# Kernel optimization log

Hardware: AMD Instinct MI355X
Metric: run time of the kernel (lower is better)

Reference implementation:

```python
import jax, jax.numpy as jnp
import numpy as np

B, L, PRED = 32, 1024, 256
CIN = 32            # enc_in == dec_in == c_out
DM, DFF, H, M = 512, 2048, 8, 64
E = DM // H
EL, DL = 2, 1
K = 25              # moving-avg kernel


def moving_avg(x):
    # torch: replicate-pad (K-1)//2 on both ends, then AvgPool1d(K, stride=1)
    pad = (K - 1) // 2
    xp = jnp.concatenate([jnp.repeat(x[:, :1], pad, axis=1), x, jnp.repeat(x[:, -1:], pad, axis=1)], axis=1)
    cs = jnp.cumsum(xp, axis=1)
    cs = jnp.concatenate([jnp.zeros_like(cs[:, :1]), cs], axis=1)
    return (cs[:, K:] - cs[:, :-K]) / K


def decomp(x):
    ma = moving_avg(x)
    return x - ma, ma


def circ_conv3(x, W):
    # Conv1d(kernel=3, padding=1, padding_mode='circular', bias=False); x:[B,L,C], W:[O,C,3]
    xp = jnp.concatenate([x[:, -1:], x, x[:, :1]], axis=1)
    win = jnp.stack([xp[:, :-2], xp[:, 1:-1], xp[:, 2:]], axis=-1)  # [B,L,C,3]
    return jnp.einsum('blcj,ocj->blo', win, W)


def pos_emb():
    pos = jnp.arange(L, dtype=jnp.float32)[:, None]
    div = jnp.exp(jnp.arange(0, DM, 2, dtype=jnp.float32) * (-np.log(10000.0) / DM))
    pe = jnp.zeros((L, DM), dtype=jnp.float32)
    pe = pe.at[:, 0::2].set(jnp.sin(pos * div))
    pe = pe.at[:, 1::2].set(jnp.cos(pos * div))
    return pe


def fourier_self(q, k, v, w):
    # FourierBlock: rFFT over time, keep lowest M modes, per-(head,mode) complex matmul, irFFT
    Bq, Lq = q.shape[0], q.shape[1]
    xft = jnp.fft.rfft(q.transpose(0, 2, 3, 1), axis=-1)[..., :M]        # [B,H,E,M]
    wc = w[..., 0] + 1j * w[..., 1]                                      # [H,E,E,M]
    om = jnp.einsum('bhem,heom->bhom', xft, wc)
    out_ft = jnp.zeros((Bq, H, E, Lq // 2 + 1), dtype=om.dtype).at[..., :M].set(om)
    return jnp.fft.irfft(out_ft, n=Lq, axis=-1).transpose(0, 3, 1, 2)    # [B,L,H,E]


def fourier_cross(q, k, v, w):
    # FourierCrossAttention (activation='tanh'); note official code uses k-modes as values
    Bq, Lq = q.shape[0], q.shape[1]
    xq = jnp.fft.rfft(q.transpose(0, 2, 3, 1), axis=-1)[..., :M]         # [B,H,E,M]
    xk = jnp.fft.rfft(k.transpose(0, 2, 3, 1), axis=-1)[..., :M]
    qk = jnp.tanh(jnp.einsum('bhex,bhey->bhxy', xq, xk))                 # complex tanh
    qkv = jnp.einsum('bhxy,bhey->bhex', qk, xk)
    wc = w[..., 0] + 1j * w[..., 1]
    om = jnp.einsum('bhex,heox->bhox', qkv, wc)
    out_ft = jnp.zeros((Bq, H, E, Lq // 2 + 1), dtype=om.dtype).at[..., :M].set(om)
    return jnp.fft.irfft(out_ft / (DM * DM), n=Lq, axis=-1).transpose(0, 3, 1, 2)


def mha(xq, xkv, Wq, bq, Wk, bk, Wv, bv, Wo, bo, inner, fw):
    Bq, Lq = xq.shape[0], xq.shape[1]
    q = (xq @ Wq.T + bq).reshape(Bq, Lq, H, E)
    k = (xkv @ Wk.T + bk).reshape(Bq, -1, H, E)
    v = (xkv @ Wv.T + bv).reshape(Bq, -1, H, E)
    o = inner(q, k, v, fw).reshape(Bq, Lq, DM)
    return o @ Wo.T + bo


def setup_inputs():
    ks = iter(jax.random.split(jax.random.key(0), 80))
    p = lambda shape: jax.random.normal(next(ks), shape, dtype=jnp.float32) * 0.02
    z = lambda shape: jnp.zeros(shape, dtype=jnp.float32)
    d = {}
    d['x_enc'] = jax.random.normal(next(ks), (B, L, CIN), dtype=jnp.float32)
    d['tok_W'] = p((DM, CIN, 3))
    for pre, n in (('enc_', EL), ('dec_s', DL), ('dec_c', DL)):
        for nm in ('Wq', 'Wk', 'Wv', 'Wo'):
            d[pre + nm] = p((n, DM, DM))
        for nm in ('bq', 'bk', 'bv', 'bo'):
            d[pre + nm] = z((n, DM))
    d['enc_c1W'] = p((EL, DFF, DM)); d['enc_c1b'] = z((EL, DFF))
    d['enc_c2W'] = p((EL, DM, DFF)); d['enc_c2b'] = z((EL, DM))
    d['dec_c1W'] = p((DL, DFF, DM)); d['dec_c1b'] = z((DL, DFF))
    d['dec_c2W'] = p((DL, DM, DFF)); d['dec_c2b'] = z((DL, DM))
    d['dec_trW'] = p((DL, CIN, DM, 3))
    d['fb_enc'] = p((H, E, E, M, 2))
    d['fb_dec'] = p((H, E, E, M, 2))
    d['fc_w'] = p((H, E, E, M, 2))
    d['p1W'] = p((CIN, CIN)); d['p1b'] = z((CIN,))
    d['p2W'] = p((PRED, L)); d['p2b'] = z((PRED,))
    d['p3W'] = p((CIN, DM)); d['p3b'] = z((CIN,))
    return d


def reference(x_enc, tok_W, enc_Wq, enc_Wk, enc_Wv, enc_Wo, enc_bq, enc_bk, enc_bv, enc_bo,
              dec_sWq, dec_sWk, dec_sWv, dec_sWo, dec_sbq, dec_sbk, dec_sbv, dec_sbo,
              dec_cWq, dec_cWk, dec_cWv, dec_cWo, dec_cbq, dec_cbk, dec_cbv, dec_cbo,
              enc_c1W, enc_c1b, enc_c2W, enc_c2b, dec_c1W, dec_c1b, dec_c2W, dec_c2b,
              dec_trW, fb_enc, fb_dec, fc_w, p1W, p1b, p2W, p2b, p3W, p3b):
    seasonal_init, trend_init = decomp(x_enc)
    enc = circ_conv3(x_enc, tok_W) + pos_emb()[None]   # DataEmbedding (eval: no dropout)
    for l in range(EL):
        h = enc + mha(enc, enc, enc_Wq[l], enc_bq[l], enc_Wk[l], enc_bk[l], enc_Wv[l], enc_bv[l],
                      enc_Wo[l], enc_bo[l], fourier_self, fb_enc)
        h, _ = decomp(h)
        y = jax.nn.relu(h @ enc_c1W[l].T + enc_c1b[l]) @ enc_c2W[l].T + enc_c2b[l]
        enc, _ = decomp(h + y)
    # NB: top-level source calls decoder(enc_out, enc_out, ...): dec_embedding output is unused
    x = enc
    trend = trend_init
    for l in range(DL):
        x = x + mha(x, x, dec_sWq[l], dec_sbq[l], dec_sWk[l], dec_sbk[l], dec_sWv[l], dec_sbv[l],
                    dec_sWo[l], dec_sbo[l], fourier_self, fb_dec)
        x, t1 = decomp(x)
        x = x + mha(x, enc, dec_cWq[l], dec_cbq[l], dec_cWk[l], dec_cbk[l], dec_cWv[l], dec_cbv[l],
                    dec_cWo[l], dec_cbo[l], fourier_cross, fc_w)
        x, t2 = decomp(x)
        y = jax.nn.relu(x @ dec_c1W[l].T + dec_c1b[l]) @ dec_c2W[l].T + dec_c2b[l]
        x, t3 = decomp(x + y)
        trend = trend + circ_conv3(t1 + t2 + t3, dec_trW[l])   # trend projection (circular conv3)
    out = trend + (x @ p3W.T + p3b)                            # [B,L,CIN]
    out = out @ p1W.T + p1b
    out = jnp.einsum('blc,pl->bpc', out, p2W) + p2b[None, :, None]  # proj2 over time -> [B,PRED,CIN]
    return out
```

## Files before the change

kernel.cpp:

```cpp
#include <hip/hip_runtime.h>
#include <math.h>

namespace {

constexpr int cB = 32, cL = 1024, cCIN = 32, cDM = 512, cDFF = 2048;
constexpr int cH = 8, cE = 64, cM = 64, cPRED = 256;
constexpr int M2 = 2 * cM;

typedef __attribute__((ext_vector_type(8))) short short8v;
typedef __attribute__((ext_vector_type(4))) float float4v;

__device__ inline unsigned short f2bf(float f) {
  unsigned int u = __builtin_bit_cast(unsigned int, f);
  u += 0x7FFFu + ((u >> 16) & 1u);
  return (unsigned short)(u >> 16);
}
__device__ inline float bf2f(unsigned short s) {
  return __builtin_bit_cast(float, (unsigned int)s << 16);
}

typedef const __attribute__((address_space(1))) unsigned int gu32_t;
typedef __attribute__((address_space(3))) unsigned int lu32_t;
__device__ inline void gld16(const void* g, void* l) {
  __builtin_amdgcn_global_load_lds((gu32_t*)g, (lu32_t*)l, 16, 0, 0);
}

__global__ void basis_kernel(short* __restrict__ basisdb, short* __restrict__ basisib) {
  int idx = blockIdx.x * 256 + threadIdx.x;
  if (idx >= M2 * cL) return;
  int t = idx & (cL - 1);
  int m2 = idx >> 10;
  int m = m2 >> 1;
  float ang = 6.2831853071795864f * (float)((m * t) & (cL - 1)) / (float)cL;
  float cv = cosf(ang), sv = sinf(ang);
  float vd = (m2 & 1) ? -sv : cv;
  basisdb[idx] = (short)f2bf(vd);
  float s = (m == 0) ? ((m2 & 1) ? 0.f : (1.f / (float)cL)) : (2.f / (float)cL);
  basisib[t * M2 + m2] = (short)f2bf(vd * s);
}

__global__ void pe_kernel(float* __restrict__ pe) {
  int idx = blockIdx.x * 256 + threadIdx.x;
  int o = idx & (cDM - 1), t = idx >> 9;
  int i = o >> 1;
  float freq = __expf((float)(2 * i) * (-9.210340371976184f / (float)cDM));
  float ang = freq * (float)t;
  pe[idx] = (o & 1) ? cosf(ang) : sinf(ang);
}

constexpr int NJOB = 14;
struct CvtArgs {
  const float* src[NJOB];
  short* dst[NJOB];
  int n[NJOB];
};
__global__ void cvtm_kernel(CvtArgs a) {
  int j = blockIdx.y;
  const float* s = a.src[j];
  short* d = a.dst[j];
  int n = a.n[j];
  for (int i = blockIdx.x * 256 + threadIdx.x; i < n; i += gridDim.x * 256)
    d[i] = (short)f2bf(s[i]);
}

__global__ void prep_kernel(const float* __restrict__ tok_W, const float* __restrict__ trW,
                            const float* __restrict__ p3W, const float* __restrict__ p3b,
                            short* __restrict__ Bpadb, short* __restrict__ Wtr3b,
                            short* __restrict__ p3padb, float* __restrict__ p3bpadf) {
  int idx = blockIdx.x * 256 + threadIdx.x;
  if (idx < 512 * 128) {
    int o = idx >> 7, s = idx & 127, j = s >> 5, c = s & 31;
    Bpadb[idx] = (j < 3) ? (short)f2bf(tok_W[o * 96 + c * 3 + j]) : (short)0;
  }
  if (idx < 128 * 1536) {
    int o = idx / 1536, r = idx % 1536, j = r >> 9, c = r & 511;
    Wtr3b[idx] = (o < 32) ? (short)f2bf(trW[(long)o * 1536 + c * 3 + j]) : (short)0;
  }
  if (idx < 128 * 512) {
    int o = idx >> 9, k = idx & 511;
    p3padb[idx] = (o < 32) ? (short)f2bf(p3W[o * 512 + k]) : (short)0;
  }
  if (idx < 128) p3bpadf[idx] = (idx < 32) ? p3b[idx] : 0.f;
}

__global__ void winbuild_kernel(const float* __restrict__ x, short* __restrict__ win) {
  int idx = blockIdx.x * 256 + threadIdx.x;
  int s4 = idx & 31;
  int row = idx >> 5;
  int t = row & (cL - 1), b = row >> 10;
  int j = s4 >> 3, c4 = s4 & 7;
  unsigned int lo = 0, hi = 0;
  if (j < 3) {
    int ts = (t + j + cL - 1) & (cL - 1);
    float4 v = *(const float4*)&x[((long)b * cL + ts) * cCIN + c4 * 4];
    lo = (unsigned int)f2bf(v.x) | ((unsigned int)f2bf(v.y) << 16);
    hi = (unsigned int)f2bf(v.z) | ((unsigned int)f2bf(v.w) << 16);
  }
  *(uint2*)&win[row * 128 + s4 * 4] = make_uint2(lo, hi);
}

__global__ __launch_bounds__(256) void transpose_bf(const short* __restrict__ in,
                                                    short* __restrict__ out) {
  __shared__ short tile[32][33];
  int b = blockIdx.z;
  in += (long)b * cL * cDM;
  out += (long)b * cL * cDM;
  int c0 = blockIdx.x * 32, t0 = blockIdx.y * 32;
  int tx = threadIdx.x & 31, ty = threadIdx.x >> 5;
#pragma unroll
  for (int r = 0; r < 32; r += 8) tile[ty + r][tx] = in[(long)(t0 + ty + r) * cDM + c0 + tx];
  __syncthreads();
#pragma unroll
  for (int r = 0; r < 32; r += 8)
    out[(long)(c0 + ty + r) * cL + t0 + tx] = tile[tx][ty + r];
}

__global__ void decomp_kernel(const float* __restrict__ x, float* __restrict__ maf, int n8,
                              int C) {
  int idx = blockIdx.x * 256 + threadIdx.x;
  if (idx >= n8) return;
  int c = idx % C;
  int u = idx / C;
  int t0 = (u & 127) * 8;
  int b = u >> 7;
  long base = (long)b * cL * C + c;
  float s = 0.f;
#pragma unroll
  for (int j = -12; j <= 12; j++) {
    int tt = t0 + j;
    tt = tt < 0 ? 0 : (tt >= cL ? cL - 1 : tt);
    s += x[base + (long)tt * C];
  }
#pragma unroll
  for (int k = 0; k < 8; k++) {
    int t = t0 + k;
    maf[base + (long)t * C] = s * (1.0f / 25.0f);
    int ta = t + 13;
    ta = ta >= cL ? cL - 1 : ta;
    int td = t - 12;
    td = td < 0 ? 0 : td;
    s += x[base + (long)ta * C] - x[base + (long)td * C];
  }
}

__global__ void decompb_kernel(const short* __restrict__ x, short* __restrict__ sb,
                               short* __restrict__ mab, int maacc, int n8, int C) {
  int idx = blockIdx.x * 256 + threadIdx.x;
  if (idx >= n8) return;
  int c = idx % C;
  int u = idx / C;
  int t0 = (u & 127) * 8;
  int b = u >> 7;
  long base = (long)b * cL * C + c;
  float s = 0.f;
#pragma unroll
  for (int j = -12; j <= 12; j++) {
    int tt = t0 + j;
    tt = tt < 0 ? 0 : (tt >= cL ? cL - 1 : tt);
    s += bf2f((unsigned short)x[base + (long)tt * C]);
  }
#pragma unroll
  for (int k = 0; k < 8; k++) {
    int t = t0 + k;
    long e = base + (long)t * C;
    float ma = s * (1.0f / 25.0f);
    if (sb) sb[e] = (short)f2bf(bf2f((unsigned short)x[e]) - ma);
    if (mab) {
      float v = maacc ? bf2f((unsigned short)mab[e]) + ma : ma;
      mab[e] = (short)f2bf(v);
    }
    int ta = t + 13;
    ta = ta >= cL ? cL - 1 : ta;
    int td = t - 12;
    td = td < 0 ? 0 : td;
    s += bf2f((unsigned short)x[base + (long)ta * C]) - bf2f((unsigned short)x[base + (long)td * C]);
  }
}

__global__ __launch_bounds__(256) void p2_kernel(const float* __restrict__ x,
                                                 const float* __restrict__ W,
                                                 const float* __restrict__ bias,
                                                 float* __restrict__ out) {
  __shared__ float tile[256 * 32];
  int b = blockIdx.x;
  int p0 = blockIdx.y * 8;
  int c = threadIdx.x & 31, pl = threadIdx.x >> 5;
  const float* xb = x + (long)b * cL * cCIN;
  const float* w = W + (long)(p0 + pl) * cL;
  float s = 0.f;
  for (int l0 = 0; l0 < cL; l0 += 256) {
    __syncthreads();
    for (int i = threadIdx.x; i < 256 * 32; i += 256) tile[i] = xb[(long)l0 * 32 + i];
    __syncthreads();
#pragma unroll 8
    for (int l = 0; l < 256; l++) s += tile[l * 32 + c] * w[l0 + l];
  }
  out[((long)b * cPRED + p0 + pl) * cCIN + c] = s + bias[p0 + pl];
}

__global__ __launch_bounds__(512) void modemix_t_kernel(const float* __restrict__ F,
                                                        const unsigned short* __restrict__ W,
                                                        short* __restrict__ Gt, float scale) {
  int b = blockIdx.x, h = blockIdx.y;
  __shared__ float2 Fs[cE][cM];
  __shared__ short ot[128][72];
  const float* Fb = F + ((long)b * cDM + h * cE) * M2;
  for (int i = threadIdx.x; i < cE * cM; i += 512) {
    int e = i >> 6, x = i & 63;
    Fs[e][x] = ((const float2*)(Fb + (long)e * M2))[x];
  }
  __syncthreads();
  int x = threadIdx.x & 63, og = threadIdx.x >> 6;
  float2 acc[8];
#pragma unroll
  for (int i = 0; i < 8; i++) acc[i] = make_float2(0.f, 0.f);
  for (int e = 0; e < cE; e++) {
    float2 f = Fs[e][x];
#pragma unroll
    for (int i = 0; i < 8; i++) {
      int o = og * 8 + i;
      unsigned int wu = *(const unsigned int*)&W[((((long)h * cE + e) * cE + o) * cM + x) * 2];
      float wx = bf2f((unsigned short)wu), wy = bf2f((unsigned short)(wu >> 16));
      acc[i].x += f.x * wx - f.y * wy;
      acc[i].y += f.x * wy + f.y * wx;
    }
  }
#pragma unroll
  for (int i = 0; i < 8; i++) {
    int o = og * 8 + i;
    ot[2 * x][o] = (short)f2bf(acc[i].x * scale);
    ot[2 * x + 1][o] = (short)f2bf(acc[i].y * scale);
  }
  __syncthreads();
  short* gb = Gt + (long)b * (M2 * cDM) + h * cE;
  for (int u = threadIdx.x; u < 1024; u += 512) {
    int row = u >> 3, seg = u & 7;
    *(uint4*)&gb[(long)row * cDM + seg * 8] = *(const uint4*)&ot[row][seg * 8];
  }
}

__global__ __launch_bounds__(1024) void fused_cross_kernel(const float* __restrict__ Fq,
                                                           const float* __restrict__ Fk,
                                                           const unsigned short* __restrict__ W,
                                                           short* __restrict__ Gt, float scale) {
  __shared__ __align__(16) char smem[65536];
  float2(*KsT)[cE] = (float2(*)[cE])smem;
  float2(*qks)[cM] = (float2(*)[cM])(smem + 32768);
  int b = blockIdx.x, h = blockIdx.y;
  const float* kb = Fk + ((long)b * cDM + h * cE) * M2;
  for (int i = threadIdx.x; i < cE * cM; i += 1024) {
    int e = i >> 6, y = i & 63;
    KsT[y][e] = ((const float2*)(kb + (long)e * M2))[y];
  }
  __syncthreads();
  {
    int x = threadIdx.x & 63, yg = threadIdx.x >> 6;
    const float* qb = Fq + ((long)b * cDM + h * cE) * M2;
    float2 acc[4];
#pragma unroll
    for (int i = 0; i < 4; i++) acc[i] = make_float2(0.f, 0.f);
    for (int e = 0; e < cE; e++) {
      float2 q = ((const float2*)(qb + (long)e * M2))[x];
#pragma unroll
      for (int i = 0; i < 4; i++) {
        float2 k = KsT[yg * 4 + i][e];
        acc[i].x += q.x * k.x - q.y * k.y;
        acc[i].y += q.x * k.y + q.y * k.x;
      }
    }
#pragma unroll
    for (int i = 0; i < 4; i++) {
      int y = yg * 4 + i;
      float a = acc[i].x, bi = acc[i].y;
      float re, im;
      float t2a = 2.f * a;
      if (fabsf(t2a) > 60.f) {
        re = t2a > 0.f ? 1.f : -1.f;
        im = 0.f;
      } else {
        float denom = coshf(t2a) + cosf(2.f * bi);
        re = sinhf(t2a) / denom;
        im = sinf(2.f * bi) / denom;
      }
      qks[y][x] = make_float2(re, im);
    }
  }
  __syncthreads();
  int e = threadIdx.x & 63, xg = threadIdx.x >> 6;
  float2 a2[4];
#pragma unroll
  for (int i = 0; i < 4; i++) a2[i] = make_float2(0.f, 0.f);
  for (int y = 0; y < cM; y++) {
    float2 k = KsT[y][e];
#pragma unroll
    for (int i = 0; i < 4; i++) {
      float2 qk = qks[y][xg * 4 + i];
      a2[i].x += qk.x * k.x - qk.y * k.y;
      a2[i].y += qk.x * k.y + qk.y * k.x;
    }
  }
  __syncthreads();
  float2(*Qv)[cM] = (float2(*)[cM])smem;
#pragma unroll
  for (int i = 0; i < 4; i++) Qv[e][xg * 4 + i] = a2[i];
  __syncthreads();
  {
    int x = threadIdx.x & 63, og = threadIdx.x >> 6;
    float2 m[4];
#pragma unroll
    for (int i = 0; i < 4; i++) m[i] = make_float2(0.f, 0.f);
    for (int ee = 0; ee < cE; ee++) {
      float2 f = Qv[ee][x];
#pragma unroll
      for (int i = 0; i < 4; i++) {
        int o = og * 4 + i;
        unsigned int wu = *(const unsigned int*)&W[((((long)h * cE + ee) * cE + o) * cM + x) * 2];
        float wx = bf2f((unsigned short)wu), wy = bf2f((unsigned short)(wu >> 16));
        m[i].x += f.x * wx - f.y * wy;
        m[i].y += f.x * wy + f.y * wx;
      }
    }
    short(*ot)[72] = (short(*)[72])(smem + 32768);
#pragma unroll
    for (int i = 0; i < 4; i++) {
      int o = og * 4 + i;
      ot[2 * x][o] = (short)f2bf(m[i].x * scale);
      ot[2 * x + 1][o] = (short)f2bf(m[i].y * scale);
    }
    __syncthreads();
    short* gb = Gt + (long)b * (M2 * cDM) + h * cE;
    int u = threadIdx.x;
    {
      int row = u >> 3, seg = u & 7;
      *(uint4*)&gb[(long)row * cDM + seg * 8] =
          *(const uint4*)&((short(*)[72])(smem + 32768))[row][seg * 8];
    }
  }
}

constexpr int GBM = 128, GBN = 128, GBK = 16, LPAD = 132;

__global__ __launch_bounds__(256) void gemm_kernel(const float* __restrict__ A,
                                                   const float* __restrict__ B,
                                                   const float* __restrict__ bias,
                                                   float* __restrict__ C, int M, int N, int K) {
  __shared__ float As[GBK][LPAD];
  __shared__ float Bs[GBK][LPAD];
  int n0 = blockIdx.x * GBN, m0 = blockIdx.y * GBM;
  int tid = threadIdx.x;
  int tx = tid & 15, ty = tid >> 4;
  float acc[8][8];
#pragma unroll
  for (int i = 0; i < 8; i++)
#pragma unroll
    for (int j = 0; j < 8; j++) acc[i][j] = 0.f;

  for (int k0 = 0; k0 < K; k0 += GBK) {
#pragma unroll
    for (int p = 0; p < 8; p++) {
      int i = p * 256 + tid;
      int mm = i >> 4, kk = i & 15;
      int gm = m0 + mm;
      As[kk][mm] = (gm < M && k0 + kk < K) ? A[(long)gm * K + k0 + kk] : 0.f;
    }
#pragma unroll
    for (int p = 0; p < 8; p++) {
      int i = p * 256 + tid;
      int nn = i >> 4, kk = i & 15;
      int gn = n0 + nn;
      Bs[kk][nn] = (gn < N && k0 + kk < K) ? B[(long)gn * K + k0 + kk] : 0.f;
    }
    __syncthreads();
#pragma unroll
    for (int kk = 0; kk < GBK; kk++) {
      float a[8], bb[8];
      *(float4*)&a[0] = *(const float4*)&As[kk][ty * 8];
      *(float4*)&a[4] = *(const float4*)&As[kk][ty * 8 + 4];
      *(float4*)&bb[0] = *(const float4*)&Bs[kk][tx * 8];
      *(float4*)&bb[4] = *(const float4*)&Bs[kk][tx * 8 + 4];
#pragma unroll
      for (int i = 0; i < 8; i++)
#pragma unroll
        for (int j = 0; j < 8; j++) acc[i][j] += a[i] * bb[j];
    }
    __syncthreads();
  }

  for (int i = 0; i < 8; i++) {
    int gm = m0 + ty * 8 + i;
    if (gm >= M) break;
    long rowoff = (long)gm * N;
    for (int j = 0; j < 8; j++) {
      int gn = n0 + tx * 8 + j;
      if (gn < N) C[rowoff + gn] = acc[i][j] + (bias ? bias[gn] : 0.f);
    }
  }
}

__global__ __launch_bounds__(256) void mfma_gemm_bf(
    const short* __restrict__ A, const short* __restrict__ B, const float* __restrict__ bias,
    const float* __restrict__ addend, const short* __restrict__ addendb,
    const float* __restrict__ pe, const float* __restrict__ m0b, float* __restrict__ Cf,
    short* __restrict__ Cb, int M, int N, int K, int lda, long sA, long sB, long sC, int relu,
    int Nreal, int ldc, int amode) {
  __shared__ __align__(16) short As[8192];
  __shared__ __align__(16) short Bs[8192];
  int nwg = gridDim.x * gridDim.y * gridDim.z;
  int orig = blockIdx.x + gridDim.x * (blockIdx.y + gridDim.y * blockIdx.z);
  int q = nwg >> 3, r = nwg & 7;
  int xcd = orig & 7, ii = orig >> 3;
  int flat = (xcd < r ? xcd * (q + 1) : r * (q + 1) + (xcd - r) * q) + ii;
  int bx = flat % (int)gridDim.x;
  int tmp = flat / (int)gridDim.x;
  int by = tmp % (int)gridDim.y;
  int bz = tmp / (int)gridDim.y;

  int z = bz;
  A += (long)z * sA;
  B += (long)z * sB;
  if (Cf) Cf += (long)z * sC;
  if (Cb) Cb += (long)z * sC;
  const float* Ad = addend ? addend + (long)z * sC : nullptr;
  const short* Adb = addendb ? addendb + (long)z * sC : nullptr;
  int n0 = bx * 128, m0 = by * 128;
  int tid = threadIdx.x;
  int lane = tid & 63;
  int w = tid >> 6;
  int wm = w & 1, wn = w >> 1;
  int lr = lane & 15, lg = lane >> 4;
  int lrow = lane >> 3;
  int scol = ((lane & 7) * 8) ^ (lrow << 3);

  float4v acc[4][4];
#pragma unroll
  for (int i = 0; i < 4; i++)
#pragma unroll
    for (int j = 0; j < 4; j++) acc[i][j] = (float4v){0.f, 0.f, 0.f, 0.f};

  auto stage = [&](int k0) {
#pragma unroll
    for (int j = 0; j < 4; j++) {
      int seg = w * 4 + j;
      int row = seg * 8 + lrow;
      const short* ga;
      if (amode == 0) {
        ga = A + (long)(m0 + row) * lda + k0 + scol;
      } else {
        int r2 = m0 + row;
        int bb = r2 >> 10, t = r2 & 1023;
        int jj = k0 >> 9, c0 = k0 & 511;
        ga = A + ((((long)(bb << 10)) | ((t + jj + 1023) & 1023)) << 9) + c0 + scol;
      }
      gld16(ga, &As[seg * 512]);
      const short* gb = B + (long)(n0 + row) * K + k0 + scol;
      gld16(gb, &Bs[seg * 512]);
    }
  };

  int nk = K >> 6;
  int swr = (lr & 7) << 3;
  for (int t = 0; t < nk; ++t) {
    stage(t << 6);
    asm volatile("s_waitcnt vmcnt(0)" ::: "memory");
    __syncthreads();
#pragma unroll
    for (int ks = 0; ks < 2; ks++) {
      short8v af[4], bfr[4];
#pragma unroll
      for (int mi = 0; mi < 4; mi++)
        af[mi] = *(const short8v*)&As[(wm * 64 + mi * 16 + lr) * 64 + ((ks * 32 + lg * 8) ^ swr)];
#pragma unroll
      for (int ni = 0; ni < 4; ni++)
        bfr[ni] = *(const short8v*)&Bs[(wn * 64 + ni * 16 + lr) * 64 + ((ks * 32 + lg * 8) ^ swr)];
#pragma unroll
      for (int mi = 0; mi < 4; mi++)
#pragma unroll
        for (int ni = 0; ni < 4; ni++)
          acc[mi][ni] =
              __builtin_amdgcn_mfma_f32_16x16x32_bf16(af[mi], bfr[ni], acc[mi][ni], 0, 0, 0);
    }
    __syncthreads();
  }

#pragma unroll
  for (int mi = 0; mi < 4; mi++) {
#pragma unroll
    for (int i = 0; i < 4; i++) {
      int gr = m0 + wm * 64 + mi * 16 + lg * 4 + i;
      long rowoff = (long)gr * ldc;
#pragma unroll
      for (int ni = 0; ni < 4; ni++) {
        int gc = n0 + wn * 64 + ni * 16 + lr;
        if (gc < Nreal) {
          float v = acc[mi][ni][i];
          if (bias) v += bias[gc];
          if (pe) v += pe[((gr & (cL - 1)) << 9) + gc];
          if (m0b && gc == 0) v += 1024.f * m0b[gr];
          if (Ad) v += Ad[rowoff + gc];
          if (Adb) v += bf2f((unsigned short)Adb[rowoff + gc]);
          if (relu) v = fmaxf(v, 0.f);
          if (Cf) Cf[rowoff + gc] = v;
          if (Cb) Cb[rowoff + gc] = (short)f2bf(v);
        }
      }
    }
  }
}

__global__ __launch_bounds__(256) void mfma_gemm64(
    const short* __restrict__ A, const short* __restrict__ B, const float* __restrict__ bias,
    const float* __restrict__ addf, const short* __restrict__ addb,
    const float* __restrict__ m0b, float* __restrict__ Cf, short* __restrict__ Cb, int M, int N,
    int K, int lda, long sA, long sB, long sC, int Nreal, int ldc, int amode,
    const short* __restrict__ A2, const short* __restrict__ B2, const float* __restrict__ m0b2,
    float* __restrict__ Cf2, int zsplit) {
  __shared__ __align__(16) short As[4096];
  __shared__ __align__(16) short Bs[4096];
  int nwg = gridDim.x * gridDim.y * gridDim.z;
  int orig = blockIdx.x + gridDim.x * (blockIdx.y + gridDim.y * blockIdx.z);
  int q = nwg >> 3, r = nwg & 7;
  int xcd = orig & 7, ii = orig >> 3;
  int flat = (xcd < r ? xcd * (q + 1) : r * (q + 1) + (xcd - r) * q) + ii;
  int bx = flat % (int)gridDim.x;
  int tmp = flat / (int)gridDim.x;
  int by = tmp % (int)gridDim.y;
  int bz = tmp / (int)gridDim.y;

  int z = bz;
  if (zsplit > 0 && bz >= zsplit) {
    A = A2;
    B = B2;
    m0b = m0b2;
    Cf = Cf2;
    z = bz - zsplit;
  }
  A += (long)z * sA;
  B += (long)z * sB;
  if (Cf) Cf += (long)z * sC;
  if (Cb) Cb += (long)z * sC;
  const float* Ad = addf ? addf + (long)z * sC : nullptr;
  const short* Adb = addb ? addb + (long)z * sC : nullptr;
  int n0 = bx * 64, m0 = by * 64;
  int tid = threadIdx.x;
  int lane = tid & 63;
  int w = tid >> 6;
  int wm = w & 1, wn = w >> 1;
  int lr = lane & 15, lg = lane >> 4;
  int lrow = lane >> 3;
  int scol = ((lane & 7) * 8) ^ (lrow << 3);

  float4v acc[2][2];
#pragma unroll
  for (int i = 0; i < 2; i++)
#pragma unroll
    for (int j = 0; j < 2; j++) acc[i][j] = (float4v){0.f, 0.f, 0.f, 0.f};

  int nk = K >> 6;
  int swr = (lr & 7) << 3;
  for (int t = 0; t < nk; ++t) {
    int k0 = t << 6;
#pragma unroll
    for (int j = 0; j < 2; j++) {
      int seg = w * 2 + j;
      int row = seg * 8 + lrow;
      const short* ga;
      if (amode == 0) {
        ga = A + (long)(m0 + row) * lda + k0 + scol;
      } else {
        int r2 = m0 + row;
        int bb = r2 >> 10, tt = r2 & 1023;
        int jj = k0 >> 9, c0 = k0 & 511;
        ga = A + ((((long)(bb << 10)) | ((tt + jj + 1023) & 1023)) << 9) + c0 + scol;
      }
      gld16(ga, &As[seg * 512]);
      gld16(B + (long)(n0 + row) * K + k0 + scol, &Bs[seg * 512]);
    }
    asm volatile("s_waitcnt vmcnt(0)" ::: "memory");
    __syncthreads();
#pragma unroll
    for (int ks = 0; ks < 2; ks++) {
      short8v af[2], bfr[2];
#pragma unroll
      for (int mi = 0; mi < 2; mi++)
        af[mi] = *(const short8v*)&As[(wm * 32 + mi * 16 + lr) * 64 + ((ks * 32 + lg * 8) ^ swr)];
#pragma unroll
      for (int ni = 0; ni < 2; ni++)
        bfr[ni] = *(const short8v*)&Bs[(wn * 32 + ni * 16 + lr) * 64 + ((ks * 32 + lg * 8) ^ swr)];
#pragma unroll
      for (int mi = 0; mi < 2; mi++)
#pragma unroll
        for (int ni = 0; ni < 2; ni++)
          acc[mi][ni] =
              __builtin_amdgcn_mfma_f32_16x16x32_bf16(af[mi], bfr[ni], acc[mi][ni], 0, 0, 0);
    }
    __syncthreads();
  }

#pragma unroll
  for (int mi = 0; mi < 2; mi++) {
#pragma unroll
    for (int i = 0; i < 4; i++) {
      int gr = m0 + wm * 32 + mi * 16 + lg * 4 + i;
      long rowoff = (long)gr * ldc;
#pragma unroll
      for (int ni = 0; ni < 2; ni++) {
        int gc = n0 + wn * 32 + ni * 16 + lr;
        if (gc < Nreal) {
          float v = acc[mi][ni][i];
          if (bias) v += bias[gc];
          if (m0b && gc == 0) v += 1024.f * m0b[gr];
          if (Ad) v += Ad[rowoff + gc];
          if (Adb) v += bf2f((unsigned short)Adb[rowoff + gc]);
          if (Cf) Cf[rowoff + gc] = v;
          if (Cb) Cb[rowoff + gc] = (short)f2bf(v);
        }
      }
    }
  }
}

}

extern "C" void kernel_launch(void* const* d_in, const int* in_sizes, int n_in, void* d_out,
                              int out_size, void* d_ws, size_t ws_size, hipStream_t stream) {
  const float* x_enc = (const float*)d_in[0];
  const float* tok_W = (const float*)d_in[1];
  const float* enc_Wq = (const float*)d_in[2];
  const float* enc_Wo = (const float*)d_in[5];
  const float* enc_bq = (const float*)d_in[6];
  const float* enc_bo = (const float*)d_in[9];
  const float* dsWq = (const float*)d_in[10];
  const float* dsWo = (const float*)d_in[13];
  const float* dsbq = (const float*)d_in[14];
  const float* dsbo = (const float*)d_in[17];
  const float* dcWq = (const float*)d_in[18];
  const float* dcWk = (const float*)d_in[19];
  const float* dcWo = (const float*)d_in[21];
  const float* dcbq = (const float*)d_in[22];
  const float* dcbk = (const float*)d_in[23];
  const float* dcbo = (const float*)d_in[25];
  const float* enc_c1W = (const float*)d_in[26];
  const float* enc_c1b = (const float*)d_in[27];
  const float* enc_c2W = (const float*)d_in[28];
  const float* enc_c2b = (const float*)d_in[29];
  const float* dec_c1W = (const float*)d_in[30];
  const float* dec_c1b = (const float*)d_in[31];
  const float* dec_c2W = (const float*)d_in[32];
  const float* dec_c2b = (const float*)d_in[33];
  const float* dec_trW = (const float*)d_in[34];
  const float* fb_enc = (const float*)d_in[35];
  const float* fb_dec = (const float*)d_in[36];
  const float* fc_w = (const float*)d_in[37];
  const float* p1W = (const float*)d_in[38];
  const float* p1b = (const float*)d_in[39];
  const float* p2W = (const float*)d_in[40];
  const float* p2b = (const float*)d_in[41];
  const float* p3W = (const float*)d_in[42];
  const float* p3b = (const float*)d_in[43];

  constexpr long MIXW = 8L * 64 * 64 * 64 * 2;

  auto layout_bytes = [&](long BG, long RH) -> size_t {
    size_t t = 0;
    auto add = [&](size_t b) { t = (t + b + 255) & ~(size_t)255; };
    add(2 * 262144 * 2); add(2 * 262144 * 2);
    add(262144 * 2); add(262144 * 2); add(262144 * 2); add(262144 * 2); add(262144 * 2);
    add(2 * 1048576 * 2); add(2 * 1048576 * 2); add(1048576 * 2); add(1048576 * 2);
    add(131072 * 2); add(131072 * 2); add(65536 * 2); add(196608 * 2); add(65536 * 2);
    add(128 * 4); add(524288 * 4);
    add(MIXW * 2); add(MIXW * 2); add(MIXW * 2);
    long GA = BG * cL * cDM;
    add(GA * 2); add(GA * 2); add(GA * 2); add(GA * 2); add(GA * 2);
    add(BG * cL * 128 * 2);
    size_t ub = (size_t)GA * 2;
    size_t hd = (size_t)RH * cDFF * 2;
    add(ub > hd ? ub : hd);
    add(BG * 65536 * 4); add(BG * 65536 * 4);
    add(BG * 65536 * 2); add(BG * 65536 * 2); add(BG * 65536 * 2); add(BG * 65536 * 2);
    add(BG * cL * cCIN * 4); add(BG * cL * cCIN * 4); add(BG * cL * cCIN * 4);
    return t;
  };
  int BG = cB;
  while (BG > 1 && layout_bytes(BG, 512) > ws_size) BG >>= 1;
  long RH = (long)BG * cL;
  while (RH > 512 && layout_bytes(BG, RH) > ws_size) RH >>= 1;

  long GBL = (long)BG * cL;
  char* base = (char*)d_ws;
  size_t off = 0;
  auto alloc = [&](size_t bytes) -> void* {
    void* p = base + off;
    off = (off + bytes + 255) & ~(size_t)255;
    return p;
  };
  short* WqbE = (short*)alloc(2 * 262144 * 2);
  short* WobE = (short*)alloc(2 * 262144 * 2);
  short* dsWqb = (short*)alloc(262144 * 2);
  short* dsWob = (short*)alloc(262144 * 2);
  short* dcWqb = (short*)alloc(262144 * 2);
  short* dcWkb = (short*)alloc(262144 * 2);
  short* dcWob = (short*)alloc(262144 * 2);
  short* c1bE = (short*)alloc(2 * 1048576 * 2);
  short* c2bE = (short*)alloc(2 * 1048576 * 2);
  short* c1bD = (short*)alloc(1048576 * 2);
  short* c2bD = (short*)alloc(1048576 * 2);
  short* basisdb = (short*)alloc(131072 * 2);
  short* basisib = (short*)alloc(131072 * 2);
  short* Bpadb = (short*)alloc(65536 * 2);
  short* Wtr3b = (short*)alloc(196608 * 2);
  short* p3padb = (short*)alloc(65536 * 2);
  float* p3bpadf = (float*)alloc(128 * 4);
  float* pe = (float*)alloc(524288 * 4);
  short* fbEb = (short*)alloc(MIXW * 2);
  short* fbDb = (short*)alloc(MIXW * 2);
  short* fcwb = (short*)alloc(MIXW * 2);
  long GA = GBL * cDM;
  short* Eb = (short*)alloc(GA * 2);
  short* Xb = (short*)alloc(GA * 2);
  short* Ab = (short*)alloc(GA * 2);
  short* Sb = (short*)alloc(GA * 2);
  short* Yb = (short*)alloc(GA * 2);
  short* winb = (short*)alloc(GBL * 128 * 2);
  size_t ubsz = (size_t)GA * 2;
  size_t hdsz = (size_t)RH * cDFF * 2;
  short* UB = (short*)alloc(ubsz > hdsz ? ubsz : hdsz);
  short* Tb = UB;
  short* HDb = UB;
  float* Fq = (float*)alloc((size_t)BG * 65536 * 4);
  float* Fk = (float*)alloc((size_t)BG * 65536 * 4);
  short* FEb = (short*)alloc((size_t)BG * 65536 * 2);
  short* FXb = (short*)alloc((size_t)BG * 65536 * 2);
  short* Gtb = (short*)alloc((size_t)BG * 65536 * 2);
  short* Hb = (short*)alloc((size_t)BG * 65536 * 2);
  float* TRD = (float*)alloc(GBL * cCIN * 4);
  float* O1 = (float*)alloc(GBL * cCIN * 4);
  float* O2 = (float*)alloc(GBL * cCIN * 4);

  auto mg = [&](const short* Am, const short* Bm, const float* bias, const float* add,
                const short* adb, const float* peA, const float* m0b, float* Cf, short* Cb,
                int Mm, int Nn, int Kk, int lda, long sA, long sB, long sC, int batch, int relu,
                int Nreal, int ldc, int amode) {
    dim3 g(Nn / 128, Mm / 128, batch);
    mfma_gemm_bf<<<g, 256, 0, stream>>>(Am, Bm, bias, add, adb, peA, m0b, Cf, Cb, Mm, Nn, Kk,
                                        lda, sA, sB, sC, relu, Nreal, ldc, amode);
  };
  auto mg64 = [&](const short* Am, const short* Bm, const float* bias, const float* addf,
                  const short* addb, const float* m0b, float* Cf, short* Cb, int Mm, int Nn,
                  int Kk, int lda, long sA, long sB, long sC, int batch, int Nreal, int ldc,
                  int amode) {
    dim3 g(Nn / 64, Mm / 64, batch);
    mfma_gemm64<<<g, 256, 0, stream>>>(Am, Bm, bias, addf, addb, m0b, Cf, Cb, Mm, Nn, Kk, lda,
                                       sA, sB, sC, Nreal, ldc, amode, nullptr, nullptr, nullptr,
                                       nullptr, 0);
  };
  auto decompf = [&](const float* x, float* maf, long total, int C_) {
    int n8 = (int)(total / 8);
    decomp_kernel<<<(n8 + 255) / 256, 256, 0, stream>>>(x, maf, n8, C_);
  };
  auto decompb = [&](const short* x, short* sb, short* mab, int maacc, long total, int C_) {
    int n8 = (int)(total / 8);
    decompb_kernel<<<(n8 + 255) / 256, 256, 0, stream>>>(x, sb, mab, maacc, n8, C_);
  };
  auto dft = [&](const short* srcb, short* Fout) {
    transpose_bf<<<dim3(16, 32, BG), 256, 0, stream>>>(srcb, Tb);
    mg64(basisdb, Tb, nullptr, nullptr, nullptr, nullptr, nullptr, Fout, M2, cDM, cL, cL, 0,
         (long)cDM * cL, 65536, BG, cDM, cDM, 0);
  };
  auto modeproj = [&](const short* Wb, const short* Fin, const float* m0b, float* Cf, short* Cb) {
    mg64(Wb, Fin, nullptr, nullptr, nullptr, m0b, Cf, Cb, cDM, M2, cDM, cDM, 0, 65536, 65536, BG,
         M2, M2, 0);
  };
  auto modeproj2 = [&](const short* Wa, const short* Fa, const float* ba, float* Ca,
                       const short* Wb2, const short* Fb2, const float* bb2, float* Cb2) {
    dim3 g(M2 / 64, cDM / 64, 2 * BG);
    mfma_gemm64<<<g, 256, 0, stream>>>(Wa, Fa, nullptr, nullptr, nullptr, ba, Ca, nullptr, cDM,
                                       M2, cDM, cDM, 0, 65536, 65536, M2, M2, 0, Wb2, Fb2, bb2,
                                       Cb2, BG);
  };
  auto idft = [&](const short* Hin, const float* bias, const short* adb, short* Cbout) {
    mg64(basisib, Hin, bias, nullptr, adb, nullptr, nullptr, Cbout, cL, cDM, M2, M2, 0, 65536,
         (long)cL * cDM, BG, cDM, cDM, 0);
  };
  auto ffn = [&](const short* inb, const short* addb, short* outb, const short* c1w,
                 const float* c1bias, const short* c2w, const float* c2bias) {
    for (long r = 0; r < GBL; r += RH) {
      mg(inb + r * cDM, c1w, c1bias, nullptr, nullptr, nullptr, nullptr, nullptr, HDb, (int)RH,
         cDFF, cDM, cDM, 0, 0, 0, 1, 1, cDFF, cDFF, 0);
      mg(HDb, c2w, c2bias, nullptr, addb + r * cDM, nullptr, nullptr, nullptr, outb + r * cDM,
         (int)RH, cDM, cDFF, cDFF, 0, 0, 0, 1, 0, cDM, cDM, 0);
    }
  };
  auto trendg = [&](const short* mab) {
    mg64(mab, Wtr3b, nullptr, TRD, nullptr, nullptr, TRD, nullptr, (int)GBL, 64, 1536, 512, 0, 0,
         0, 1, cCIN, cCIN, 1);
  };
  auto mixt = [&](const float* F, const short* W, float scale) {
    modemix_t_kernel<<<dim3(BG, cH), 512, 0, stream>>>(F, (const unsigned short*)W, Gtb, scale);
  };

  basis_kernel<<<(M2 * cL) / 256, 256, 0, stream>>>(basisdb, basisib);
  pe_kernel<<<(cL * cDM) / 256, 256, 0, stream>>>(pe);
  prep_kernel<<<768, 256, 0, stream>>>(tok_W, dec_trW, p3W, p3b, Bpadb, Wtr3b, p3padb, p3bpadf);
  {
    CvtArgs ca;
    const float* srcs[NJOB] = {enc_Wq, enc_Wo, dsWq, dsWo, dcWq, dcWk, dcWo,
                               enc_c1W, enc_c2W, dec_c1W, dec_c2W, fb_enc, fb_dec, fc_w};
    short* dsts[NJOB] = {WqbE, WobE, dsWqb, dsWob, dcWqb, dcWkb, dcWob,
                         c1bE, c2bE, c1bD, c2bD, fbEb, fbDb, fcwb};
    int ns[NJOB] = {524288, 524288, 262144, 262144, 262144, 262144, 262144,
                    2097152, 2097152, 1048576, 1048576, (int)MIXW, (int)MIXW, (int)MIXW};
    for (int j = 0; j < NJOB; j++) {
      ca.src[j] = srcs[j];
      ca.dst[j] = dsts[j];
      ca.n[j] = ns[j];
    }
    cvtm_kernel<<<dim3(256, NJOB), 256, 0, stream>>>(ca);
  }

  for (int b0 = 0; b0 < cB; b0 += BG) {
    const float* xg = x_enc + (long)b0 * cL * cCIN;

    decompf(xg, TRD, GBL * cCIN, cCIN);
    winbuild_kernel<<<(int)(GBL * 32 / 256), 256, 0, stream>>>(xg, winb);
    mg(winb, Bpadb, nullptr, nullptr, nullptr, pe, nullptr, nullptr, Eb, (int)GBL, cDM, 128, 128,
       0, 0, 0, 1, 0, cDM, cDM, 0);

    for (int l = 0; l < 2; l++) {
      dft(Eb, FEb);
      modeproj(WqbE + (long)l * 262144, FEb, enc_bq + l * cDM, Fq, nullptr);
      mixt(Fq, fbEb, 1.0f);
      modeproj(WobE + (long)l * 262144, Gtb, nullptr, nullptr, Hb);
      idft(Hb, enc_bo + l * cDM, Eb, Yb);
      decompb(Yb, Xb, nullptr, 0, GA, cDM);
      ffn(Xb, Xb, Yb, c1bE + (long)l * 1048576, enc_c1b + l * cDFF, c2bE + (long)l * 1048576,
          enc_c2b + l * cDM);
      decompb(Yb, Eb, nullptr, 0, GA, cDM);
    }

    dft(Eb, FEb);
    modeproj(dsWqb, FEb, dsbq, Fq, nullptr);
    mixt(Fq, fbDb, 1.0f);
    modeproj(dsWob, Gtb, nullptr, nullptr, Hb);
    idft(Hb, dsbo, Eb, Yb);
    decompb(Yb, Xb, Sb, 0, GA, cDM);
    dft(Xb, FXb);
    modeproj2(dcWqb, FXb, dcbq, Fq, dcWkb, FEb, dcbk, Fk);
    fused_cross_kernel<<<dim3(BG, cH), 1024, 0, stream>>>(Fq, Fk, (const unsigned short*)fcwb,
                                                          Gtb, 1.0f / (float)(cDM * cDM));
    modeproj(dcWob, Gtb, nullptr, nullptr, Hb);
    idft(Hb, dcbo, Xb, Yb);
    decompb(Yb, Ab, Sb, 1, GA, cDM);
    ffn(Ab, Ab, Yb, c1bD, dec_c1b, c2bD, dec_c2b);
    decompb(Yb, Xb, Sb, 1, GA, cDM);
    trendg(Sb);

    mg64(Xb, p3padb, p3bpadf, TRD, nullptr, nullptr, O1, nullptr, (int)GBL, 64, cDM, cDM, 0, 0,
         0, 1, cCIN, cCIN, 0);
    gemm_kernel<<<dim3(1, (int)(GBL / 128)), 256, 0, stream>>>(O1, p1W, p1b, O2, (int)GBL, cCIN,
                                                               cCIN);
    p2_kernel<<<dim3(BG, 32), 256, 0, stream>>>(O2, p2W, p2b,
                                                (float*)d_out + (long)b0 * cPRED * cCIN);
  }
}
```

Before: 2.184 ms.

## Replace 128x128 GEMM with 256x128 tile, 512-thread MFMA kernel for FFN and embedding

Replaces the general batched 128x128-tile bf16 MFMA GEMM with a specialized kernel that uses 256x128 output tiles and 8 waves (512 threads). The batch, amode, fp32 addend, m0b and Nreal bounds paths are removed. Larger M tiles let each B tile loaded into LDS be reused across twice as many rows, which cuts global traffic per FLOP in the FFN and embedding GEMMs. The cost is more LDS per block, fewer blocks in the grid and possibly lower occupancy, and it assumes M is divisible by 256 and N by 128.

```diff
diff --git a/kernel.cpp b/kernel.cpp
--- a/kernel.cpp
+++ b/kernel.cpp
@@ -397,36 +397,26 @@
   }
 }
 
-__global__ __launch_bounds__(256) void mfma_gemm_bf(
+__global__ __launch_bounds__(512) void mfma_gemm256(
     const short* __restrict__ A, const short* __restrict__ B, const float* __restrict__ bias,
-    const float* __restrict__ addend, const short* __restrict__ addendb,
-    const float* __restrict__ pe, const float* __restrict__ m0b, float* __restrict__ Cf,
-    short* __restrict__ Cb, int M, int N, int K, int lda, long sA, long sB, long sC, int relu,
-    int Nreal, int ldc, int amode) {
-  __shared__ __align__(16) short As[8192];
+    const short* __restrict__ addendb, const float* __restrict__ pe, float* __restrict__ Cf,
+    short* __restrict__ Cb, int M, int N, int K, int lda, int relu, int ldc) {
+  __shared__ __align__(16) short As[16384];
   __shared__ __align__(16) short Bs[8192];
-  int nwg = gridDim.x * gridDim.y * gridDim.z;
-  int orig = blockIdx.x + gridDim.x * (blockIdx.y + gridDim.y * blockIdx.z);
+  int nwg = gridDim.x * gridDim.y;
+  int orig = blockIdx.x + gridDim.x * blockIdx.y;
   int q = nwg >> 3, r = nwg & 7;
   int xcd = orig & 7, ii = orig >> 3;
   int flat = (xcd < r ? xcd * (q + 1) : r * (q + 1) + (xcd - r) * q) + ii;
   int bx = flat % (int)gridDim.x;
-  int tmp = flat / (int)gridDim.x;
-  int by = tmp % (int)gridDim.y;
-  int bz = tmp / (int)gridDim.y;
-
-  int z = bz;
-  A += (long)z * sA;
-  B += (long)z * sB;
-  if (Cf) Cf += (long)z * sC;
-  if (Cb) Cb += (long)z * sC;
-  const float* Ad = addend ? addend + (long)z * sC : nullptr;
-  const short* Adb = addendb ? addendb + (long)z * sC : nullptr;
-  int n0 = bx * 128, m0 = by * 128;
+  int by = flat / (int)gridDim.x;
+
+  int n0 = bx * 128, m0 = by * 256;
   int tid = threadIdx.x;
   int lane = tid & 63;
   int w = tid >> 6;
-  int wm = w & 1, wn = w >> 1;
+  int wm = w >> 1;
+  int wn = w & 1;
   int lr = lane & 15, lg = lane >> 4;
   int lrow = lane >> 3;
   int scol = ((lane & 7) * 8) ^ (lrow << 3);
@@ -437,30 +427,22 @@
 #pragma unroll
     for (int j = 0; j < 4; j++) acc[i][j] = (float4v){0.f, 0.f, 0.f, 0.f};
 
-  auto stage = [&](int k0) {
+  int nk = K >> 6;
+  int swr = (lr & 7) << 3;
+  for (int t = 0; t < nk; ++t) {
+    int k0 = t << 6;
 #pragma unroll
     for (int j = 0; j < 4; j++) {
       int seg = w * 4 + j;
       int row = seg * 8 + lrow;
-      const short* ga;
-      if (amode == 0) {
-        ga = A + (long)(m0 + row) * lda + k0 + scol;
-      } else {
-        int r2 = m0 + row;
-        int bb = r2 >> 10, t = r2 & 1023;
-        int jj = k0 >> 9, c0 = k0 & 511;
-        ga = A + ((((long)(bb << 10)) | ((t + jj + 1023) & 1023)) << 9) + c0 + scol;
-      }
-      gld16(ga, &As[seg * 512]);
-      const short* gb = B + (long)(n0 + row) * K + k0 + scol;
-      gld16(gb, &Bs[seg * 512]);
-    }
-  };
-
-  int nk = K >> 6;
-  int swr = (lr & 7) << 3;
-  for (int t = 0; t < nk; ++t) {
-    stage(t << 6);
+      gld16(A + (long)(m0 + row) * lda + k0 + scol, &As[seg * 512]);
+    }
+#pragma unroll
+    for (int j = 0; j < 2; j++) {
+      int seg = w * 2 + j;
+      int row = seg * 8 + lrow;
+      gld16(B + (long)(n0 + row) * K + k0 + scol, &Bs[seg * 512]);
+    }
     asm volatile("s_waitcnt vmcnt(0)" ::: "memory");
     __syncthreads();
 #pragma unroll
@@ -491,17 +473,13 @@
 #pragma unroll
       for (int ni = 0; ni < 4; ni++) {
         int gc = n0 + wn * 64 + ni * 16 + lr;
-        if (gc < Nreal) {
-          float v = acc[mi][ni][i];
-          if (bias) v += bias[gc];
-          if (pe) v += pe[((gr & (cL - 1)) << 9) + gc];
-          if (m0b && gc == 0) v += 1024.f * m0b[gr];
-          if (Ad) v += Ad[rowoff + gc];
-          if (Adb) v += bf2f((unsigned short)Adb[rowoff + gc]);
-          if (relu) v = fmaxf(v, 0.f);
-          if (Cf) Cf[rowoff + gc] = v;
-          if (Cb) Cb[rowoff + gc] = (short)f2bf(v);
-        }
+        float v = acc[mi][ni][i];
+        if (bias) v += bias[gc];
+        if (pe) v += pe[((gr & (cL - 1)) << 9) + gc];
+        if (addendb) v += bf2f((unsigned short)addendb[rowoff + gc]);
+        if (relu) v = fmaxf(v, 0.f);
+        if (Cf) Cf[rowoff + gc] = v;
+        if (Cb) Cb[rowoff + gc] = (short)f2bf(v);
       }
     }
   }
@@ -736,13 +714,12 @@
   float* O1 = (float*)alloc(GBL * cCIN * 4);
   float* O2 = (float*)alloc(GBL * cCIN * 4);
 
-  auto mg = [&](const short* Am, const short* Bm, const float* bias, const float* add,
-                const short* adb, const float* peA, const float* m0b, float* Cf, short* Cb,
-                int Mm, int Nn, int Kk, int lda, long sA, long sB, long sC, int batch, int relu,
-                int Nreal, int ldc, int amode) {
-    dim3 g(Nn / 128, Mm / 128, batch);
-    mfma_gemm_bf<<<g, 256, 0, stream>>>(Am, Bm, bias, add, adb, peA, m0b, Cf, Cb, Mm, Nn, Kk,
-                                        lda, sA, sB, sC, relu, Nreal, ldc, amode);
+  auto mg256 = [&](const short* Am, const short* Bm, const float* bias, const short* adb,
+                   const float* peA, float* Cf, short* Cb, int Mm, int Nn, int Kk, int lda,
+                   int relu, int ldc) {
+    dim3 g(Nn / 128, Mm / 256);
+    mfma_gemm256<<<g, 512, 0, stream>>>(Am, Bm, bias, adb, peA, Cf, Cb, Mm, Nn, Kk, lda, relu,
+                                        ldc);
   };
   auto mg64 = [&](const short* Am, const short* Bm, const float* bias, const float* addf,
                   const short* addb, const float* m0b, float* Cf, short* Cb, int Mm, int Nn,
@@ -784,10 +761,10 @@
   auto ffn = [&](const short* inb, const short* addb, short* outb, const short* c1w,
                  const float* c1bias, const short* c2w, const float* c2bias) {
     for (long r = 0; r < GBL; r += RH) {
-      mg(inb + r * cDM, c1w, c1bias, nullptr, nullptr, nullptr, nullptr, nullptr, HDb, (int)RH,
-         cDFF, cDM, cDM, 0, 0, 0, 1, 1, cDFF, cDFF, 0);
-      mg(HDb, c2w, c2bias, nullptr, addb + r * cDM, nullptr, nullptr, nullptr, outb + r * cDM,
-         (int)RH, cDM, cDFF, cDFF, 0, 0, 0, 1, 0, cDM, cDM, 0);
+      mg256(inb + r * cDM, c1w, c1bias, nullptr, nullptr, nullptr, HDb, (int)RH, cDFF, cDM, cDM,
+            1, cDFF);
+      mg256(HDb, c2w, c2bias, addb + r * cDM, nullptr, nullptr, outb + r * cDM, (int)RH, cDM,
+            cDFF, cDFF, 0, cDM);
     }
   };
   auto trendg = [&](const short* mab) {
@@ -822,8 +799,7 @@
 
     decompf(xg, TRD, GBL * cCIN, cCIN);
     winbuild_kernel<<<(int)(GBL * 32 / 256), 256, 0, stream>>>(xg, winb);
-    mg(winb, Bpadb, nullptr, nullptr, nullptr, pe, nullptr, nullptr, Eb, (int)GBL, cDM, 128, 128,
-       0, 0, 0, 1, 0, cDM, cDM, 0);
+    mg256(winb, Bpadb, nullptr, nullptr, pe, nullptr, Eb, (int)GBL, cDM, 128, 128, 0, cDM);
 
     for (int l = 0; l < 2; l++) {
       dft(Eb, FEb);
```

Result: faster. 2.101 ms (-3.8%).
